# Kernel tuning notes

Measured on AMD Instinct MI355X. Metric: run time of the kernel, lower is better.

## Reference

```python
import jax, jax.numpy as jnp
import numpy as np

B, DIN, DK, DV, H, DOUT = 16384, 2048, 2048, 2048, 16, 512
dk, dv = DK // H, DV // H  # 128, 128

def setup_inputs() -> dict:
    key = jax.random.key(0)
    ks = jax.random.split(key, 10)
    s_in = 1.0 / np.sqrt(DIN)
    s_v = 1.0 / np.sqrt(DV)
    s_2in = 1.0 / np.sqrt(2 * DIN)
    return {
        "x": jax.random.normal(ks[0], (B, DIN), jnp.float32),
        "Wq": jax.random.normal(ks[1], (DIN, DK), jnp.float32) * s_in,
        "Wk": jax.random.normal(ks[2], (DIN, DK), jnp.float32) * s_in,
        "Wv": jax.random.normal(ks[3], (DIN, DV), jnp.float32) * s_in,
        "Wo": jax.random.normal(ks[4], (DV, DIN), jnp.float32) * s_v,
        "bo": jax.random.normal(ks[5], (DIN,), jnp.float32) * s_v,
        "Wg": jax.random.normal(ks[6], (2 * DIN, DIN), jnp.float32) * s_2in,
        "bg": jax.random.normal(ks[7], (DIN,), jnp.float32) * s_2in,
        "Wout": jax.random.normal(ks[8], (DIN, DOUT), jnp.float32) * s_in,
        "bout": jax.random.normal(ks[9], (DOUT,), jnp.float32) * s_in,
    }

def _feat(t):
    # kernel feature map: relu(x) + 1e-4
    return jax.nn.relu(t) + 1e-4

def reference(x, Wq, Wk, Wv, Wo, bo, Wg, bg, Wout, bout):
    b = x.shape[0]
    q = _feat((x @ Wq).reshape(b, H, dk))
    k = _feat((x @ Wk).reshape(b, H, dk))
    v = (x @ Wv).reshape(b, H, dv)
    # linear attention: aggregate over batch (acts as sequence)
    kv = jnp.einsum('bhd,bhe->hde', k, v)            # [H, dk, dv]
    z = 1.0 / (jnp.einsum('bhd,hd->bh', q, k.sum(axis=0)) + 1e-6)  # [B, H]
    att = jnp.einsum('bhd,hde->bhe', q, kv) * z[..., None]         # [B, H, dv]
    att = att.reshape(b, DV)
    out_proj = att @ Wo + bo
    gate = jax.nn.sigmoid(jnp.concatenate([out_proj, x], axis=-1) @ Wg + bg)
    out = gate * out_proj + (1.0 - gate) * x
    return out @ Wout + bout
```

## Files before the change

### kernel.cpp

```cpp
#include <hip/hip_runtime.h>
#include <hip/hip_bf16.h>
#include <math.h>

typedef __bf16 bf16_t;
typedef __attribute__((ext_vector_type(8))) __bf16 bf16x8;
typedef __attribute__((ext_vector_type(4))) __bf16 bf16x4;
typedef __attribute__((ext_vector_type(16))) float f32x16;

#define DEVI __device__ __forceinline__

constexpr int B_SZ = 16384, DIN = 2048, DK = 2048, DV = 2048, NH = 16, DOUT = 512;

DEVI void load_lds16(const void* gptr, void* lptr) {
  __builtin_amdgcn_global_load_lds(
      (const __attribute__((address_space(1))) unsigned int*)gptr,
      (__attribute__((address_space(3))) unsigned int*)lptr,
      16, 0, 0);
}

template <int EPI>
__global__ __launch_bounds__(256, 4) void gemm_bt(
    const bf16_t* __restrict__ A, int lda, long aZ,
    const bf16_t* __restrict__ Bt, int ldb, long bZ,
    void* __restrict__ Cv, int ldc, long cZ, int K,
    const float* __restrict__ aux1,
    const float* __restrict__ aux2) {
  __shared__ __align__(16) bf16_t As[2][128 * 32];
  __shared__ __align__(16) bf16_t Bs[2][128 * 32];
  const int tid = threadIdx.x;
  const int bn = blockIdx.x, bm = blockIdx.y, bz = blockIdx.z;
  const int lane = tid & 63, w = tid >> 6;
  const int wm = (w & 1) * 64, wn = (w >> 1) * 64;
  const int lm = lane & 31, lh = lane >> 5;

  const bf16_t* __restrict__ Ab = A + (long)bm * 128 * lda + (long)bz * aZ;
  const bf16_t* __restrict__ Bb = Bt + (long)bn * 128 * ldb + (long)bz * bZ;

  const int srow = tid >> 2, scol = (tid & 3) * 8;
  const long aRow = (long)srow * lda + scol;
  const long bRow = (long)srow * ldb + scol;

  const char* aBase = (const char*)As + (wm + lm) * 64 + lh * 16;
  const char* bBase = (const char*)Bs + (wn + lm) * 64 + lh * 16;

  f32x16 acc[2][2] = {};

  for (int k0 = 0; k0 < K; k0 += 64) {
    const bf16_t* ap = Ab + aRow + k0;
    const bf16_t* bp = Bb + bRow + k0;
    load_lds16(ap, &As[0][tid * 8]);
    load_lds16(ap + (long)64 * lda, &As[0][2048 + tid * 8]);
    load_lds16(ap + 32, &As[1][tid * 8]);
    load_lds16(ap + (long)64 * lda + 32, &As[1][2048 + tid * 8]);
    load_lds16(bp, &Bs[0][tid * 8]);
    load_lds16(bp + (long)64 * ldb, &Bs[0][2048 + tid * 8]);
    load_lds16(bp + 32, &Bs[1][tid * 8]);
    load_lds16(bp + (long)64 * ldb + 32, &Bs[1][2048 + tid * 8]);
    __syncthreads();
#pragma unroll
    for (int s = 0; s < 4; ++s) {
      const int off = (s >> 1) * 8192 + (s & 1) * 32;
      const bf16x8 af0 = *(const bf16x8*)(aBase + off);
      const bf16x8 af1 = *(const bf16x8*)(aBase + off + 2048);
      const bf16x8 bf0 = *(const bf16x8*)(bBase + off);
      const bf16x8 bf1 = *(const bf16x8*)(bBase + off + 2048);
      acc[0][0] = __builtin_amdgcn_mfma_f32_32x32x16_bf16(af0, bf0, acc[0][0], 0, 0, 0);
      acc[0][1] = __builtin_amdgcn_mfma_f32_32x32x16_bf16(af0, bf1, acc[0][1], 0, 0, 0);
      acc[1][0] = __builtin_amdgcn_mfma_f32_32x32x16_bf16(af1, bf0, acc[1][0], 0, 0, 0);
      acc[1][1] = __builtin_amdgcn_mfma_f32_32x32x16_bf16(af1, bf1, acc[1][1], 0, 0, 0);
    }
    __syncthreads();
  }

#pragma unroll
  for (int i = 0; i < 2; ++i) {
#pragma unroll
    for (int j = 0; j < 2; ++j) {
      const int col = bn * 128 + wn + j * 32 + lm;
#pragma unroll
      for (int r = 0; r < 16; ++r) {
        const int row = bm * 128 + wm + i * 32 + (r & 3) + 8 * (r >> 2) + 4 * lh;
        const long cidx = (long)row * ldc + (long)bz * cZ + col;
        float val = acc[i][j][r];
        if (EPI == 0) {
          ((bf16_t*)Cv)[cidx] = (bf16_t)val;
        } else if (EPI == 1) {
          if (col < 4096) val = fmaxf(val, 0.f) + 1e-4f;
          ((bf16_t*)Cv)[cidx] = (bf16_t)val;
        } else if (EPI == 2) {
          val += aux1[col];
          ((bf16_t*)Cv)[cidx] = (bf16_t)val;
        } else if (EPI == 4) {
          const float g = 1.f / (1.f + __expf(-(val + aux1[col])));
          const float op = (float)A[(long)row * lda + col];
          const float xx = aux2[(long)row * DIN + col];
          ((bf16_t*)Cv)[cidx] = (bf16_t)(g * op + (1.f - g) * xx);
        } else if (EPI == 5) {
          ((float*)Cv)[cidx] = val + aux1[col];
        }
      }
    }
  }
}

__global__ __launch_bounds__(256) void prep_kernel(
    const float* __restrict__ x, const float* __restrict__ Wq,
    const float* __restrict__ Wk, const float* __restrict__ Wv,
    const float* __restrict__ Wo, const float* __restrict__ Wg,
    const float* __restrict__ Wout, bf16_t* __restrict__ concat,
    bf16_t* __restrict__ WqkvT, bf16_t* __restrict__ WoT,
    bf16_t* __restrict__ WgT, bf16_t* __restrict__ WoutT) {
  const int tid = threadIdx.x;
  int b = blockIdx.x;
  if (b < 32768) {
    const long i = ((long)b * 256 + tid) * 4;
    const long row = i >> 11;
    const int col = (int)(i & 2047);
    const float4 f = *(const float4*)&x[i];
    bf16x4 o;
    o[0] = (bf16_t)f.x; o[1] = (bf16_t)f.y; o[2] = (bf16_t)f.z; o[3] = (bf16_t)f.w;
    *(bf16x4*)&concat[row * 4096 + 2048 + col] = o;
    return;
  }
  b -= 32768;
  const float* in; bf16_t* out; int R, C;
  if (b < 4096)       { in = Wq;   out = WqkvT;                     R = 2048; C = 2048; }
  else if (b < 8192)  { in = Wk;   out = WqkvT + (size_t)2048*2048; R = 2048; C = 2048; b -= 4096; }
  else if (b < 12288) { in = Wv;   out = WqkvT + (size_t)4096*2048; R = 2048; C = 2048; b -= 8192; }
  else if (b < 16384) { in = Wo;   out = WoT;                       R = 2048; C = 2048; b -= 12288; }
  else if (b < 24576) { in = Wg;   out = WgT;                       R = 4096; C = 2048; b -= 16384; }
  else                { in = Wout; out = WoutT;                     R = 2048; C = 512;  b -= 24576; }
  const int CB = C / 32;
  const int c0 = (b % CB) * 32, r0 = (b / CB) * 32;
  __shared__ bf16_t tile[32][33];
  const int tx = tid & 31, ty = tid >> 5;
  for (int i = ty; i < 32; i += 8)
    tile[i][tx] = (bf16_t)in[(long)(r0 + i) * C + c0 + tx];
  __syncthreads();
  for (int i = ty; i < 32; i += 8)
    out[(long)(c0 + i) * R + r0 + tx] = tile[tx][i];
}

__global__ __launch_bounds__(256) void ksum_kernel(const bf16_t* __restrict__ qkv,
                                                   float* __restrict__ ksum) {
  const int col = blockIdx.x * 256 + threadIdx.x;
  const int r0 = blockIdx.y * 256;
  const bf16_t* k = qkv + 2048;
  float s = 0.f;
  for (int r = 0; r < 256; ++r) s += (float)k[(long)(r0 + r) * 6144 + col];
  atomicAdd(&ksum[col], s);
}

__global__ __launch_bounds__(256) void kv_kernel(const bf16_t* __restrict__ qkv,
                                                 float* __restrict__ P) {
  const int h = blockIdx.x, sp = blockIdx.y;
  const int t = threadIdx.x;
  __shared__ __align__(16) bf16_t kS[64 * 128];
  __shared__ __align__(16) bf16_t vS[64 * 128];
  const int d0 = (t >> 4) * 8, e0 = (t & 15) * 8;
  const int srow = t >> 4, scol = (t & 15) * 8;
  float acc[8][8] = {};
  const bf16_t* kp = qkv + 2048 + h * 128;
  const bf16_t* vp = qkv + 4096 + h * 128;
  const long base = (long)sp * 512 * 6144;
  for (int c0 = 0; c0 < 512; c0 += 64) {
#pragma unroll
    for (int it = 0; it < 4; ++it) {
      load_lds16(kp + base + (long)(c0 + it * 16 + srow) * 6144 + scol, &kS[it * 2048 + t * 8]);
      load_lds16(vp + base + (long)(c0 + it * 16 + srow) * 6144 + scol, &vS[it * 2048 + t * 8]);
    }
    __syncthreads();
    for (int bb = 0; bb < 64; ++bb) {
      const bf16x8 kk = *(const bf16x8*)&kS[bb * 128 + d0];
      const bf16x8 vv = *(const bf16x8*)&vS[bb * 128 + e0];
      float kf[8], vf[8];
#pragma unroll
      for (int r = 0; r < 8; ++r) { kf[r] = (float)kk[r]; vf[r] = (float)vv[r]; }
#pragma unroll
      for (int a = 0; a < 8; ++a)
#pragma unroll
        for (int b2 = 0; b2 < 8; ++b2) acc[a][b2] += kf[a] * vf[b2];
    }
    __syncthreads();
  }
  float* Ph = P + (long)h * 16384;
#pragma unroll
  for (int a = 0; a < 8; ++a)
#pragma unroll
    for (int b2 = 0; b2 < 8; ++b2)
      atomicAdd(&Ph[(d0 + a) * 128 + e0 + b2], acc[a][b2]);
}

__global__ __launch_bounds__(256) void cvt_bf(const float* __restrict__ P,
                                              bf16_t* __restrict__ o, int n) {
  const int i = blockIdx.x * 256 + threadIdx.x;
  if (i < n) o[i] = (bf16_t)P[i];
}

__global__ __launch_bounds__(256) void z_kernel(bf16_t* __restrict__ qkv,
                                                const float* __restrict__ ksum) {
  __shared__ float ks[2048];
  const int t = threadIdx.x;
  for (int i = t; i < 2048; i += 256) ks[i] = ksum[i];
  __syncthreads();
  const int b = blockIdx.x * 16 + (t >> 4);
  const int h = t & 15;
  bf16_t* qr = qkv + (long)b * 6144 + h * 128;
  bf16x8 qq[16];
  float s = 0.f;
#pragma unroll
  for (int i = 0; i < 16; ++i) {
    qq[i] = *(const bf16x8*)&qr[i * 8];
#pragma unroll
    for (int r = 0; r < 8; ++r) s += (float)qq[i][r] * ks[h * 128 + i * 8 + r];
  }
  const float z = 1.f / (s + 1e-6f);
#pragma unroll
  for (int i = 0; i < 16; ++i) {
#pragma unroll
    for (int r = 0; r < 8; ++r) qq[i][r] = (bf16_t)((float)qq[i][r] * z);
    *(bf16x8*)&qr[i * 8] = qq[i];
  }
}

extern "C" void kernel_launch(void* const* d_in, const int* in_sizes, int n_in,
                              void* d_out, int out_size, void* d_ws, size_t ws_size,
                              hipStream_t stream) {
  const float* x    = (const float*)d_in[0];
  const float* Wq   = (const float*)d_in[1];
  const float* Wk   = (const float*)d_in[2];
  const float* Wv   = (const float*)d_in[3];
  const float* Wo   = (const float*)d_in[4];
  const float* bo   = (const float*)d_in[5];
  const float* Wg   = (const float*)d_in[6];
  const float* bg   = (const float*)d_in[7];
  const float* Wout = (const float*)d_in[8];
  const float* bout = (const float*)d_in[9];

  char* ws = (char*)d_ws;
  size_t off = 0;
  auto alloc = [&](size_t bytes) -> void* {
    void* p = ws + off;
    off += (bytes + 255) & ~(size_t)255;
    return p;
  };
  bf16_t* concat = (bf16_t*)alloc((size_t)B_SZ * 4096 * 2);
  bf16_t* qkv    = (bf16_t*)alloc((size_t)B_SZ * 6144 * 2);
  bf16_t* outb   = (bf16_t*)alloc((size_t)B_SZ * DIN * 2);
  bf16_t* WqkvT  = (bf16_t*)alloc((size_t)6144 * DIN * 2);
  bf16_t* WoT    = (bf16_t*)alloc((size_t)DIN * DV * 2);
  bf16_t* WgT    = (bf16_t*)alloc((size_t)DIN * 4096 * 2);
  bf16_t* WoutT  = (bf16_t*)alloc((size_t)DOUT * DIN * 2);
  float*  P      = (float*)alloc((size_t)NH * 128 * 128 * 4);
  bf16_t* kvbf   = (bf16_t*)alloc((size_t)NH * 128 * 128 * 2);
  bf16_t* G      = (bf16_t*)alloc((size_t)DIN * DK * 2);
  float*  ksum   = (float*)alloc((size_t)DK * 4);

  hipMemsetAsync(P, 0, (size_t)NH * 128 * 128 * 4, stream);
  hipMemsetAsync(ksum, 0, (size_t)DK * 4, stream);

  prep_kernel<<<32768 + 25600, 256, 0, stream>>>(x, Wq, Wk, Wv, Wo, Wg, Wout,
                                                 concat, WqkvT, WoT, WgT, WoutT);

  const bf16_t* xb = concat + 2048;

  gemm_bt<1><<<dim3(48, 128, 1), 256, 0, stream>>>(xb, 4096, 0, WqkvT, 2048, 0,
                                                   qkv, 6144, 0, 2048, nullptr, nullptr);

  ksum_kernel<<<dim3(8, 64), 256, 0, stream>>>(qkv, ksum);
  kv_kernel<<<dim3(16, 32), 256, 0, stream>>>(qkv, P);
  cvt_bf<<<1024, 256, 0, stream>>>(P, kvbf, NH * 128 * 128);
  z_kernel<<<B_SZ / 16, 256, 0, stream>>>(qkv, ksum);

  gemm_bt<0><<<dim3(1, 16, 16), 256, 0, stream>>>(WoT, 2048, 128, kvbf, 128, 16384,
                                                  G, 2048, 128, 128, nullptr, nullptr);

  gemm_bt<2><<<dim3(16, 128, 1), 256, 0, stream>>>(qkv, 6144, 0, G, 2048, 0,
                                                   concat, 4096, 0, 2048, bo, nullptr);

  gemm_bt<4><<<dim3(16, 128, 1), 256, 0, stream>>>(concat, 4096, 0, WgT, 4096, 0,
                                                   outb, 2048, 0, 4096, bg, x);

  gemm_bt<5><<<dim3(4, 128, 1), 256, 0, stream>>>(outb, 2048, 0, WoutT, 2048, 0,
                                                  d_out, 512, 0, 2048, bout, nullptr);
}
```

Baseline: 1.733 ms.

## Add 256x256 pipelined GEMM kernel with swizzled LDS for large projections

```diff
diff --git a/kernel.cpp b/kernel.cpp
--- a/kernel.cpp
+++ b/kernel.cpp
@@ -19,67 +19,115 @@
 }
 
 template <int EPI>
-__global__ __launch_bounds__(256, 4) void gemm_bt(
+__global__ __launch_bounds__(512, 2) void gemm256(
     const bf16_t* __restrict__ A, int lda, long aZ,
     const bf16_t* __restrict__ Bt, int ldb, long bZ,
     void* __restrict__ Cv, int ldc, long cZ, int K,
     const float* __restrict__ aux1,
     const float* __restrict__ aux2) {
-  __shared__ __align__(16) bf16_t As[2][128 * 32];
-  __shared__ __align__(16) bf16_t Bs[2][128 * 32];
+  __shared__ __align__(16) bf16_t lds[2][2][256 * 64];
   const int tid = threadIdx.x;
-  const int bn = blockIdx.x, bm = blockIdx.y, bz = blockIdx.z;
+  const int gx = gridDim.x;
+  const int nwg = gx * gridDim.y;
+  int flat = blockIdx.y * gx + blockIdx.x;
+  flat = (flat & 7) * (nwg >> 3) + (flat >> 3);
+  const int bn = flat % gx, bm = flat / gx;
+  const int bz = blockIdx.z;
+
   const int lane = tid & 63, w = tid >> 6;
-  const int wm = (w & 1) * 64, wn = (w >> 1) * 64;
+  const int wr = w >> 2, wc = w & 3;
   const int lm = lane & 31, lh = lane >> 5;
 
-  const bf16_t* __restrict__ Ab = A + (long)bm * 128 * lda + (long)bz * aZ;
-  const bf16_t* __restrict__ Bb = Bt + (long)bn * 128 * ldb + (long)bz * bZ;
-
-  const int srow = tid >> 2, scol = (tid & 3) * 8;
-  const long aRow = (long)srow * lda + scol;
-  const long bRow = (long)srow * ldb + scol;
-
-  const char* aBase = (const char*)As + (wm + lm) * 64 + lh * 16;
-  const char* bBase = (const char*)Bs + (wn + lm) * 64 + lh * 16;
-
-  f32x16 acc[2][2] = {};
-
-  for (int k0 = 0; k0 < K; k0 += 64) {
-    const bf16_t* ap = Ab + aRow + k0;
-    const bf16_t* bp = Bb + bRow + k0;
-    load_lds16(ap, &As[0][tid * 8]);
-    load_lds16(ap + (long)64 * lda, &As[0][2048 + tid * 8]);
-    load_lds16(ap + 32, &As[1][tid * 8]);
-    load_lds16(ap + (long)64 * lda + 32, &As[1][2048 + tid * 8]);
-    load_lds16(bp, &Bs[0][tid * 8]);
-    load_lds16(bp + (long)64 * ldb, &Bs[0][2048 + tid * 8]);
-    load_lds16(bp + 32, &Bs[1][tid * 8]);
-    load_lds16(bp + (long)64 * ldb + 32, &Bs[1][2048 + tid * 8]);
-    __syncthreads();
-#pragma unroll
-    for (int s = 0; s < 4; ++s) {
-      const int off = (s >> 1) * 8192 + (s & 1) * 32;
-      const bf16x8 af0 = *(const bf16x8*)(aBase + off);
-      const bf16x8 af1 = *(const bf16x8*)(aBase + off + 2048);
-      const bf16x8 bf0 = *(const bf16x8*)(bBase + off);
-      const bf16x8 bf1 = *(const bf16x8*)(bBase + off + 2048);
-      acc[0][0] = __builtin_amdgcn_mfma_f32_32x32x16_bf16(af0, bf0, acc[0][0], 0, 0, 0);
-      acc[0][1] = __builtin_amdgcn_mfma_f32_32x32x16_bf16(af0, bf1, acc[0][1], 0, 0, 0);
-      acc[1][0] = __builtin_amdgcn_mfma_f32_32x32x16_bf16(af1, bf0, acc[1][0], 0, 0, 0);
-      acc[1][1] = __builtin_amdgcn_mfma_f32_32x32x16_bf16(af1, bf1, acc[1][1], 0, 0, 0);
-    }
-    __syncthreads();
-  }
-
-#pragma unroll
-  for (int i = 0; i < 2; ++i) {
+  const bf16_t* __restrict__ Ab = A + (long)bm * 256 * lda + (long)bz * aZ;
+  const bf16_t* __restrict__ Bb = Bt + (long)bn * 256 * ldb + (long)bz * bZ;
+
+  const int srow = tid >> 3;
+  const int sslot = (tid & 7) ^ (srow & 7);
+  const long aOff = (long)srow * lda + sslot * 8;
+  const long bOff = (long)srow * ldb + sslot * 8;
+  char* const ldsc = (char*)&lds[0][0][0];
+
+  const int xorv = lm & 7;
+  const int rbA = (wr * 128 + lm) * 128;
+  const int rbB = (wc * 64 + lm) * 128 + 32768;
+  int sl16[4];
+#pragma unroll
+  for (int s = 0; s < 4; ++s) sl16[s] = (((2 * s) | lh) ^ xorv) * 16;
+
+  auto stageA = [&](int buf, int t, int h) {
+    const bf16_t* p = Ab + aOff + t * 64 + (long)h * 128 * lda;
+    char* d = ldsc + buf * 65536 + h * 16384 + tid * 16;
+    load_lds16(p, d);
+    load_lds16(p + (long)64 * lda, d + 8192);
+  };
+  auto stageB = [&](int buf, int t, int h) {
+    const bf16_t* p = Bb + bOff + t * 64 + (long)h * 128 * ldb;
+    char* d = ldsc + buf * 65536 + 32768 + h * 16384 + tid * 16;
+    load_lds16(p, d);
+    load_lds16(p + (long)64 * ldb, d + 8192);
+  };
+
+  f32x16 acc[4][2] = {};
+  const int NT = K >> 6;
+
+  stageA(0, 0, 0); stageA(0, 0, 1); stageB(0, 0, 0); stageB(0, 0, 1);
+  if (NT > 1) {
+    stageB(1, 1, 0); stageB(1, 1, 1);
+    asm volatile("s_waitcnt vmcnt(4)" ::: "memory");
+  } else {
+    asm volatile("s_waitcnt vmcnt(0)" ::: "memory");
+  }
+  __builtin_amdgcn_sched_barrier(0);
+  __builtin_amdgcn_s_barrier();
+
+  for (int t = 0; t < NT; ++t) {
+    const int cur = t & 1;
+    const char* base = ldsc + cur * 65536;
+    bf16x8 bq[2][4];
+#pragma unroll
+    for (int m = 0; m < 4; ++m) {
+      bf16x8 af[4];
+#pragma unroll
+      for (int s = 0; s < 4; ++s)
+        af[s] = *(const bf16x8*)(base + rbA + m * 4096 + sl16[s]);
+      if (m == 0) {
+#pragma unroll
+        for (int j = 0; j < 2; ++j)
+#pragma unroll
+          for (int s = 0; s < 4; ++s)
+            bq[j][s] = *(const bf16x8*)(base + rbB + j * 4096 + sl16[s]);
+      }
+      if (m == 0) { if (t + 1 < NT) stageA(cur ^ 1, t + 1, 0); }
+      if (m == 1) { if (t + 1 < NT) stageA(cur ^ 1, t + 1, 1); }
+      if (m == 2) { if (t + 2 < NT) stageB(cur, t + 2, 0); }
+      if (m == 3) { if (t + 2 < NT) stageB(cur, t + 2, 1); }
+      __builtin_amdgcn_s_barrier();
+      __builtin_amdgcn_s_setprio(1);
+#pragma unroll
+      for (int s = 0; s < 4; ++s) {
+        acc[m][0] = __builtin_amdgcn_mfma_f32_32x32x16_bf16(af[s], bq[0][s], acc[m][0], 0, 0, 0);
+        acc[m][1] = __builtin_amdgcn_mfma_f32_32x32x16_bf16(af[s], bq[1][s], acc[m][1], 0, 0, 0);
+      }
+      __builtin_amdgcn_s_setprio(0);
+      if (m == 3) {
+        if (t + 2 < NT) asm volatile("s_waitcnt vmcnt(4) lgkmcnt(0)" ::: "memory");
+        else            asm volatile("s_waitcnt vmcnt(0) lgkmcnt(0)" ::: "memory");
+      } else {
+        asm volatile("s_waitcnt lgkmcnt(0)" ::: "memory");
+      }
+      __builtin_amdgcn_sched_barrier(0);
+      __builtin_amdgcn_s_barrier();
+    }
+  }
+
+#pragma unroll
+  for (int i = 0; i < 4; ++i) {
 #pragma unroll
     for (int j = 0; j < 2; ++j) {
-      const int col = bn * 128 + wn + j * 32 + lm;
+      const int col = bn * 256 + wc * 64 + j * 32 + lm;
 #pragma unroll
       for (int r = 0; r < 16; ++r) {
-        const int row = bm * 128 + wm + i * 32 + (r & 3) + 8 * (r >> 2) + 4 * lh;
+        const int row = bm * 256 + wr * 128 + i * 32 + (r & 3) + 8 * (r >> 2) + 4 * lh;
         const long cidx = (long)row * ldc + (long)bz * cZ + col;
         float val = acc[i][j][r];
         if (EPI == 0) {
@@ -103,6 +151,80 @@
   }
 }
 
+template <int EPI>
+__global__ __launch_bounds__(256, 4) void gemm_bt(
+    const bf16_t* __restrict__ A, int lda, long aZ,
+    const bf16_t* __restrict__ Bt, int ldb, long bZ,
+    void* __restrict__ Cv, int ldc, long cZ, int K,
+    const float* __restrict__ aux1,
+    const float* __restrict__ aux2) {
+  __shared__ __align__(16) bf16_t As[2][128 * 32];
+  __shared__ __align__(16) bf16_t Bs[2][128 * 32];
+  const int tid = threadIdx.x;
+  const int bn = blockIdx.x, bm = blockIdx.y, bz = blockIdx.z;
+  const int lane = tid & 63, w = tid >> 6;
+  const int wm = (w & 1) * 64, wn = (w >> 1) * 64;
+  const int lm = lane & 31, lh = lane >> 5;
+
+  const bf16_t* __restrict__ Ab = A + (long)bm * 128 * lda + (long)bz * aZ;
+  const bf16_t* __restrict__ Bb = Bt + (long)bn * 128 * ldb + (long)bz * bZ;
+
+  const int srow = tid >> 2, scol = (tid & 3) * 8;
+  const long aRow = (long)srow * lda + scol;
+  const long bRow = (long)srow * ldb + scol;
+
+  const char* aBase = (const char*)As + (wm + lm) * 64 + lh * 16;
+  const char* bBase = (const char*)Bs + (wn + lm) * 64 + lh * 16;
+
+  f32x16 acc[2][2] = {};
+
+  for (int k0 = 0; k0 < K; k0 += 64) {
+    const bf16_t* ap = Ab + aRow + k0;
+    const bf16_t* bp = Bb + bRow + k0;
+    load_lds16(ap, &As[0][tid * 8]);
+    load_lds16(ap + (long)64 * lda, &As[0][2048 + tid * 8]);
+    load_lds16(ap + 32, &As[1][tid * 8]);
+    load_lds16(ap + (long)64 * lda + 32, &As[1][2048 + tid * 8]);
+    load_lds16(bp, &Bs[0][tid * 8]);
+    load_lds16(bp + (long)64 * ldb, &Bs[0][2048 + tid * 8]);
+    load_lds16(bp + 32, &Bs[1][tid * 8]);
+    load_lds16(bp + (long)64 * ldb + 32, &Bs[1][2048 + tid * 8]);
+    __syncthreads();
+#pragma unroll
+    for (int s = 0; s < 4; ++s) {
+      const int off = (s >> 1) * 8192 + (s & 1) * 32;
+      const bf16x8 af0 = *(const bf16x8*)(aBase + off);
+      const bf16x8 af1 = *(const bf16x8*)(aBase + off + 2048);
+      const bf16x8 bf0 = *(const bf16x8*)(bBase + off);
+      const bf16x8 bf1 = *(const bf16x8*)(bBase + off + 2048);
+      acc[0][0] = __builtin_amdgcn_mfma_f32_32x32x16_bf16(af0, bf0, acc[0][0], 0, 0, 0);
+      acc[0][1] = __builtin_amdgcn_mfma_f32_32x32x16_bf16(af0, bf1, acc[0][1], 0, 0, 0);
+      acc[1][0] = __builtin_amdgcn_mfma_f32_32x32x16_bf16(af1, bf0, acc[1][0], 0, 0, 0);
+      acc[1][1] = __builtin_amdgcn_mfma_f32_32x32x16_bf16(af1, bf1, acc[1][1], 0, 0, 0);
+    }
+    __syncthreads();
+  }
+
+#pragma unroll
+  for (int i = 0; i < 2; ++i) {
+#pragma unroll
+    for (int j = 0; j < 2; ++j) {
+      const int col = bn * 128 + wn + j * 32 + lm;
+#pragma unroll
+      for (int r = 0; r < 16; ++r) {
+        const int row = bm * 128 + wm + i * 32 + (r & 3) + 8 * (r >> 2) + 4 * lh;
+        const long cidx = (long)row * ldc + (long)bz * cZ + col;
+        float val = acc[i][j][r];
+        if (EPI == 0) {
+          ((bf16_t*)Cv)[cidx] = (bf16_t)val;
+        } else if (EPI == 5) {
+          ((float*)Cv)[cidx] = val + aux1[col];
+        }
+      }
+    }
+  }
+}
+
 __global__ __launch_bounds__(256) void prep_kernel(
     const float* __restrict__ x, const float* __restrict__ Wq,
     const float* __restrict__ Wk, const float* __restrict__ Wv,
@@ -264,8 +386,8 @@
 
   const bf16_t* xb = concat + 2048;
 
-  gemm_bt<1><<<dim3(48, 128, 1), 256, 0, stream>>>(xb, 4096, 0, WqkvT, 2048, 0,
-                                                   qkv, 6144, 0, 2048, nullptr, nullptr);
+  gemm256<1><<<dim3(24, 64, 1), 512, 0, stream>>>(xb, 4096, 0, WqkvT, 2048, 0,
+                                                  qkv, 6144, 0, 2048, nullptr, nullptr);
 
   ksum_kernel<<<dim3(8, 64), 256, 0, stream>>>(qkv, ksum);
   kv_kernel<<<dim3(16, 32), 256, 0, stream>>>(qkv, P);
@@ -275,11 +397,11 @@
   gemm_bt<0><<<dim3(1, 16, 16), 256, 0, stream>>>(WoT, 2048, 128, kvbf, 128, 16384,
                                                   G, 2048, 128, 128, nullptr, nullptr);
 
-  gemm_bt<2><<<dim3(16, 128, 1), 256, 0, stream>>>(qkv, 6144, 0, G, 2048, 0,
-                                                   concat, 4096, 0, 2048, bo, nullptr);
-
-  gemm_bt<4><<<dim3(16, 128, 1), 256, 0, stream>>>(concat, 4096, 0, WgT, 4096, 0,
-                                                   outb, 2048, 0, 4096, bg, x);
+  gemm256<2><<<dim3(8, 64, 1), 512, 0, stream>>>(qkv, 6144, 0, G, 2048, 0,
+                                                 concat, 4096, 0, 2048, bo, nullptr);
+
+  gemm256<4><<<dim3(8, 64, 1), 512, 0, stream>>>(concat, 4096, 0, WgT, 4096, 0,
+                                                 outb, 2048, 0, 4096, bg, x);
 
   gemm_bt<5><<<dim3(4, 128, 1), 256, 0, stream>>>(outb, 2048, 0, WoutT, 2048, 0,
                                                   d_out, 512, 0, 2048, bout, nullptr);
```

Measured after the change: 1.569 ms. -9.5%, faster.
